# Kernel optimization log

Measured on AMD Instinct MI355X. Metric: run time of the kernel, lower is better.

## Reference

```python
import jax, jax.numpy as jnp
import numpy as np

B, D, N_CLASSES = 8192, 128, 50


def setup_inputs() -> dict:
    key = jax.random.key(0)
    k1, k2, k3 = jax.random.split(key, 3)
    anchor = jax.random.normal(k1, (B, D), dtype=jnp.float32)
    target = jax.random.normal(k2, (B, D), dtype=jnp.float32)
    labels = jax.random.randint(k3, (B,), 0, N_CLASSES)
    return {"anchor": anchor, "target": target, "labels": labels}


def reference(anchor, target, labels):
    # Faithful vectorization of QuadrupletLoss.nt_xent_loss.
    # Note: the original hardcodes temperature 0.05 (ignores self.temp).
    TEMP = 0.05
    n = labels.shape[0]
    diff = labels[:, None] != labels[None, :]                      # mask2: [B,B]
    same_off = (labels[:, None] == labels[None, :]) & ~jnp.eye(n, dtype=bool)  # mask

    # d[j, m] = <anchor[j], target[m]> / 0.05
    d = jnp.matmul(anchor, target.T) / TEMP                        # [B,B]
    neg = jnp.where(diff, d, -jnp.inf)
    mx = jax.lax.stop_gradient(jnp.max(neg, axis=1))               # maxdot.detach() per j
    mx = jnp.where(jnp.isfinite(mx), mx, 0.0)
    # s[j] = sum_{m: labels[m]!=labels[j]} exp(d[j,m] - mx[j])  (exp(-inf)=0 masks out)
    s = jnp.sum(jnp.exp(neg - mx[:, None]), axis=1)                # [B]

    # Inner double loop: nds[i] = sum over j with labels[j]!=labels[i] of s[j]
    difff = diff.astype(s.dtype)
    nds = difff @ s                                                # [B]
    negcount = jnp.sum(difff, axis=1)                              # negtivesum

    x = jnp.where(negcount > 0, nds / jnp.where(negcount > 0, negcount, 1.0), nds)
    log_prob = -jnp.log(x + 1e-12)                                 # constant across cols
    mask_sum = jnp.sum(same_off, axis=1)
    # (mask * log_prob).sum(1) / clamp(mask_sum,1) == log_prob where mask_sum>0 else 0
    pos_logits = jnp.where(mask_sum > 0, log_prob, 0.0)
    return -jnp.mean(pos_logits)
```

## Files before the change

### kernel.cpp

```cpp
#include <hip/hip_runtime.h>
#include <float.h>
#include <math.h>

typedef __attribute__((ext_vector_type(8))) short short8;
typedef __attribute__((ext_vector_type(8))) _Float16 half8;
typedef __attribute__((ext_vector_type(4))) float f32x4;

constexpr int B_N  = 8192;
constexpr int D_KK = 128;
constexpr int NCLS = 50;
constexpr int NCHUNK = 16;
constexpr int CCOLS = B_N / NCHUNK;
constexpr int NPBLK = 32;
constexpr float C_SCALE = 28.853900817779268f;
constexpr float THR = 40.0f;
constexpr float NEG_LOW  = -1.0e5f;
constexpr float NEG_MASK = -1.0e30f;

__device__ __forceinline__ float exp2fast(float x) { return __builtin_amdgcn_exp2f(x); }

__global__ void prep_kernel(const float* __restrict__ a, const float* __restrict__ b,
                            short* __restrict__ aH, short* __restrict__ bT)
{
    const int NPER = B_N * D_KK / 8;
    int i = blockIdx.x * blockDim.x + threadIdx.x;
    if (i < NPER) {
        const f32x4* sp = (const f32x4*)(a + (size_t)i * 8);
        f32x4 v0 = sp[0], v1 = sp[1];
        short8 h;
#pragma unroll
        for (int e = 0; e < 4; ++e) {
            h[e]     = __builtin_bit_cast(short, (_Float16)(C_SCALE * v0[e]));
            h[e + 4] = __builtin_bit_cast(short, (_Float16)(C_SCALE * v1[e]));
        }
        *(short8*)(aH + (size_t)i * 8) = h;
    } else {
        int j   = i - NPER;
        int kq  = j & 15;
        int col = j >> 4;
        const f32x4* sp = (const f32x4*)(b + (size_t)col * D_KK + kq * 8);
        f32x4 v0 = sp[0], v1 = sp[1];
        short8 h;
#pragma unroll
        for (int e = 0; e < 4; ++e) {
            h[e]     = __builtin_bit_cast(short, (_Float16)v0[e]);
            h[e + 4] = __builtin_bit_cast(short, (_Float16)v1[e]);
        }
        *(short8*)(bT + (size_t)kq * B_N * 8 + (size_t)col * 8) = h;
    }
}

__global__ __launch_bounds__(256)
void rowstats_kernel(const short* __restrict__ aH, const short* __restrict__ bT,
                     const int* __restrict__ labels,
                     float* __restrict__ pmx, float* __restrict__ ps)
{
    const int bid   = blockIdx.x;
    const int chunk = bid & (NCHUNK - 1);
    const int R0    = (bid >> 4) * 128;
    const int C0    = chunk * CCOLS;

    const int tid = threadIdx.x;
    const int wid = tid >> 6, l = tid & 63;
    const int l15 = l & 15, l16 = l >> 4;
    const int wrow = R0 + wid * 32;

    half8 aF[2][4];
#pragma unroll
    for (int mf = 0; mf < 2; ++mf) {
        const int arow = wrow + mf * 16 + l15;
#pragma unroll
        for (int ks = 0; ks < 4; ++ks)
            aF[mf][ks] = __builtin_bit_cast(half8,
                *(const short8*)(aH + (size_t)arow * D_KK + ks * 32 + l16 * 8));
    }

    int labA[8];
#pragma unroll
    for (int mf = 0; mf < 2; ++mf)
#pragma unroll
        for (int r = 0; r < 4; ++r)
            labA[mf * 4 + r] = labels[wrow + mf * 16 + l16 * 4 + r];

    float mxr[8], sm[8], ref[8];
#pragma unroll
    for (int i = 0; i < 8; ++i) { mxr[i] = NEG_LOW; sm[i] = 0.0f; ref[i] = 0.0f; }

    const char* cb = (const char*)(bT + (size_t)C0 * 8);
    int vo[2][4];
#pragma unroll
    for (int nf = 0; nf < 2; ++nf)
#pragma unroll
        for (int ks = 0; ks < 4; ++ks)
            vo[nf][ks] = ((ks * 4 + l16) * B_N + nf * 16 + l15) * 16;

    const int NT = CCOLS / 32;

    half8 bF[2][4];
#pragma unroll
    for (int nf = 0; nf < 2; ++nf)
#pragma unroll
        for (int ks = 0; ks < 4; ++ks)
            bF[nf][ks] = __builtin_bit_cast(half8, *(const short8*)(cb + vo[nf][ks]));

#pragma unroll 1
    for (int t = 0; t < NT; ++t) {
        f32x4 acc[2][2];
#pragma unroll
        for (int mf = 0; mf < 2; ++mf)
#pragma unroll
            for (int nf = 0; nf < 2; ++nf)
#pragma unroll
                for (int r = 0; r < 4; ++r) acc[mf][nf][r] = -ref[mf * 4 + r];

#pragma unroll
        for (int ks = 0; ks < 4; ++ks)
#pragma unroll
            for (int mf = 0; mf < 2; ++mf)
#pragma unroll
                for (int nf = 0; nf < 2; ++nf)
                    acc[mf][nf] = __builtin_amdgcn_mfma_f32_16x16x32_f16(
                        aF[mf][ks], bF[nf][ks], acc[mf][nf], 0, 0, 0);

        if (t + 1 < NT) {
            const int off = (t + 1) * 512;
#pragma unroll
            for (int nf = 0; nf < 2; ++nf)
#pragma unroll
                for (int ks = 0; ks < 4; ++ks)
                    bF[nf][ks] = __builtin_bit_cast(half8,
                        *(const short8*)(cb + vo[nf][ks] + off));
        }

        const int colB = C0 + t * 32;
        const int lB0 = labels[colB + l15];
        const int lB1 = labels[colB + 16 + l15];

        float vm0[8], vm1[8];
        int trig = 0;
#pragma unroll
        for (int mf = 0; mf < 2; ++mf)
#pragma unroll
            for (int r = 0; r < 4; ++r) {
                const int i = mf * 4 + r;
                float v0 = (lB0 != labA[i]) ? acc[mf][0][r] : NEG_MASK;
                float v1 = (lB1 != labA[i]) ? acc[mf][1][r] : NEG_MASK;
                mxr[i] = fmaxf(fmaxf(mxr[i], v0), v1);
                vm0[i] = v0; vm1[i] = v1;
                trig |= (mxr[i] > THR) ? 1 : 0;
            }
        if (__any(trig)) {
#pragma unroll
            for (int i = 0; i < 8; ++i) {
                float dlt = fmaxf(mxr[i], 0.0f);
                sm[i] *= exp2fast(-dlt);
                ref[i] += dlt; mxr[i] -= dlt;
                vm0[i] -= dlt; vm1[i] -= dlt;
            }
        }
#pragma unroll
        for (int i = 0; i < 8; ++i)
            sm[i] += exp2fast(vm0[i]) + exp2fast(vm1[i]);
    }

    float mxa[8], so[8];
#pragma unroll
    for (int i = 0; i < 8; ++i) {
        mxa[i] = ref[i] + mxr[i];
        so[i]  = sm[i] * exp2fast(fminf(-mxr[i], 126.0f));
    }
#pragma unroll
    for (int i = 0; i < 8; ++i) {
#pragma unroll
        for (int off = 1; off < 16; off <<= 1) {
            float m2 = __shfl_xor(mxa[i], off);
            float s2 = __shfl_xor(so[i], off);
            float nm = fmaxf(mxa[i], m2);
            so[i] = so[i] * exp2fast(mxa[i] - nm) + s2 * exp2fast(m2 - nm);
            mxa[i] = nm;
        }
    }
    if (l15 == 0) {
#pragma unroll
        for (int mf = 0; mf < 2; ++mf)
#pragma unroll
            for (int r = 0; r < 4; ++r) {
                int row = wrow + mf * 16 + l16 * 4 + r;
                pmx[chunk * B_N + row] = mxa[mf * 4 + r];
                ps [chunk * B_N + row] = so[mf * 4 + r];
            }
    }
}

__global__ void classsum_kernel(const float* __restrict__ pmx, const float* __restrict__ ps,
                                const int* __restrict__ labels,
                                float* __restrict__ partSum, unsigned int* __restrict__ partCnt)
{
    __shared__ float        csL[NCLS];
    __shared__ unsigned int ccL[NCLS];
    int t = threadIdx.x;
    if (t < NCLS) { csL[t] = 0.0f; ccL[t] = 0u; }
    __syncthreads();

    int j = blockIdx.x * blockDim.x + t;
    float m = -FLT_MAX, s = 0.0f;
#pragma unroll 4
    for (int c = 0; c < NCHUNK; ++c) {
        float m2 = pmx[(size_t)c * B_N + j];
        float s2 = ps [(size_t)c * B_N + j];
        float nm = fmaxf(m, m2);
        s = s * exp2fast(m - nm) + s2 * exp2fast(m2 - nm);
        m = nm;
    }
    int lab = labels[j];
    atomicAdd(&csL[lab], s);
    atomicAdd(&ccL[lab], 1u);
    __syncthreads();
    if (t < NCLS) {
        partSum[blockIdx.x * NCLS + t] = csL[t];
        partCnt[blockIdx.x * NCLS + t] = ccL[t];
    }
}

__global__ void loss_kernel(const float* __restrict__ partSum,
                            const unsigned int* __restrict__ partCnt,
                            float* __restrict__ out)
{
    int c = threadIdx.x;
    float cs = 0.0f;
    unsigned int cc = 0u;
    if (c < NCLS) {
#pragma unroll 4
        for (int b = 0; b < NPBLK; ++b) {
            cs += partSum[b * NCLS + c];
            cc += partCnt[b * NCLS + c];
        }
    }

    float tot = cs;
#pragma unroll
    for (int off = 1; off < 64; off <<= 1) tot += __shfl_xor(tot, off);

    float contrib = 0.0f;
    if (c < NCLS && cc > 0u) {
        float negc = (float)(B_N - (int)cc);
        float nds  = tot - cs;
        float x    = (negc > 0.0f) ? (nds / negc) : nds;
        float lp   = (cc >= 2u) ? (-logf(x + 1e-12f)) : 0.0f;
        contrib = (float)cc * lp;
    }
#pragma unroll
    for (int off = 1; off < 64; off <<= 1) contrib += __shfl_xor(contrib, off);
    if (c == 0) out[0] = -(contrib / (float)B_N);
}

extern "C" void kernel_launch(void* const* d_in, const int* in_sizes, int n_in,
                              void* d_out, int out_size, void* d_ws, size_t ws_size,
                              hipStream_t stream)
{
    const float* anchor = (const float*)d_in[0];
    const float* target = (const float*)d_in[1];
    const int*   labels = (const int*)d_in[2];
    float* out = (float*)d_out;

    const size_t PLANE = (size_t)B_N * D_KK * sizeof(short);
    char* ws = (char*)d_ws;
    short* aH = (short*)(ws + 0 * PLANE);
    short* bT = (short*)(ws + 1 * PLANE);
    float* ps  = (float*)(ws + 2 * PLANE);
    float* pmx = (float*)(ws + 2 * PLANE + sizeof(float) * NCHUNK * B_N);
    char*  cls = ws + 2 * PLANE + 2 * sizeof(float) * NCHUNK * B_N;
    float*        partSum = (float*)cls;
    unsigned int* partCnt = (unsigned int*)(cls + NPBLK * NCLS * sizeof(float));

    prep_kernel<<<2 * (B_N * D_KK / 8) / 256, 256, 0, stream>>>(anchor, target, aH, bT);
    rowstats_kernel<<<(B_N / 128) * NCHUNK, 256, 0, stream>>>(aH, bT, labels, pmx, ps);
    classsum_kernel<<<B_N / 256, 256, 0, stream>>>(pmx, ps, labels, partSum, partCnt);
    loss_kernel<<<1, 64, 0, stream>>>(partSum, partCnt, out);
}
```

Measured before the change: 54.60 us.

## Fold label mask into GEMM via one-hot augmented K dimension

The K dimension grows from 128 to 192 by appending a one-hot label block: anchor rows carry -4096 at their label's slot and target columns carry 1.0, so same-label dot products are pushed far negative by the MFMA itself. This removes the per-tile label loads and compare/select masking in the rowstats loop. The running rescale offset now seeds the MFMA accumulator as a bias, the column loop is partially unrolled, and the final merge becomes a max reduction followed by a sum reduction. The cost is 50% more MFMA work and B-tile loads per tile, plus more prep work and a larger workspace.

```diff
diff --git a/kernel.cpp b/kernel.cpp
--- a/kernel.cpp
+++ b/kernel.cpp
@@ -7,52 +7,76 @@
 typedef __attribute__((ext_vector_type(4))) float f32x4;
 
 constexpr int B_N  = 8192;
-constexpr int D_KK = 128;
+constexpr int D_K  = 128;
+constexpr int K_AUG = 192;
+constexpr int NKQ  = K_AUG / 8;
 constexpr int NCLS = 50;
 constexpr int NCHUNK = 16;
-constexpr int CCOLS = B_N / NCHUNK;
+constexpr int CCOLS = 512;
 constexpr int NPBLK = 32;
 constexpr float C_SCALE = 28.853900817779268f;
-constexpr float THR = 40.0f;
-constexpr float NEG_LOW  = -1.0e5f;
-constexpr float NEG_MASK = -1.0e30f;
+constexpr float PEN  = 4096.0f;
+constexpr float THR  = 40.0f;
+constexpr float NEG_LOW = -1.0e5f;
 
 __device__ __forceinline__ float exp2fast(float x) { return __builtin_amdgcn_exp2f(x); }
 
 __global__ void prep_kernel(const float* __restrict__ a, const float* __restrict__ b,
+                            const int* __restrict__ labels,
                             short* __restrict__ aH, short* __restrict__ bT)
 {
-    const int NPER = B_N * D_KK / 8;
+    const int NA = B_N * NKQ;
     int i = blockIdx.x * blockDim.x + threadIdx.x;
-    if (i < NPER) {
-        const f32x4* sp = (const f32x4*)(a + (size_t)i * 8);
-        f32x4 v0 = sp[0], v1 = sp[1];
+    if (i < NA) {
+        int row = i / NKQ, kq = i - row * NKQ;
         short8 h;
-#pragma unroll
-        for (int e = 0; e < 4; ++e) {
-            h[e]     = __builtin_bit_cast(short, (_Float16)(C_SCALE * v0[e]));
-            h[e + 4] = __builtin_bit_cast(short, (_Float16)(C_SCALE * v1[e]));
-        }
-        *(short8*)(aH + (size_t)i * 8) = h;
-    } else {
-        int j   = i - NPER;
-        int kq  = j & 15;
-        int col = j >> 4;
-        const f32x4* sp = (const f32x4*)(b + (size_t)col * D_KK + kq * 8);
-        f32x4 v0 = sp[0], v1 = sp[1];
-        short8 h;
-#pragma unroll
-        for (int e = 0; e < 4; ++e) {
-            h[e]     = __builtin_bit_cast(short, (_Float16)v0[e]);
-            h[e + 4] = __builtin_bit_cast(short, (_Float16)v1[e]);
-        }
-        *(short8*)(bT + (size_t)kq * B_N * 8 + (size_t)col * 8) = h;
+        if (kq < 16) {
+            const f32x4* sp = (const f32x4*)(a + (size_t)row * D_K + kq * 8);
+            f32x4 v0 = sp[0], v1 = sp[1];
+#pragma unroll
+            for (int e = 0; e < 4; ++e) {
+                h[e]     = __builtin_bit_cast(short, (_Float16)(C_SCALE * v0[e]));
+                h[e + 4] = __builtin_bit_cast(short, (_Float16)(C_SCALE * v1[e]));
+            }
+        } else {
+            int lab = labels[row];
+            int base = (kq - 16) * 8;
+#pragma unroll
+            for (int e = 0; e < 8; ++e)
+                h[e] = __builtin_bit_cast(short, (lab == base + e) ? (_Float16)(-PEN)
+                                                                   : (_Float16)0.0f);
+        }
+        *(short8*)(aH + (size_t)row * K_AUG + kq * 8) = h;
+    } else if (i < NA + B_N) {
+        int col = i - NA;
+        int lab = labels[col];
+#pragma unroll 4
+        for (int kq = 0; kq < 16; ++kq) {
+            const f32x4* sp = (const f32x4*)(b + (size_t)col * D_K + kq * 8);
+            f32x4 v0 = sp[0], v1 = sp[1];
+            short8 h;
+#pragma unroll
+            for (int e = 0; e < 4; ++e) {
+                h[e]     = __builtin_bit_cast(short, (_Float16)v0[e]);
+                h[e + 4] = __builtin_bit_cast(short, (_Float16)v1[e]);
+            }
+            *(short8*)(bT + ((size_t)kq * B_N + col) * 8) = h;
+        }
+#pragma unroll
+        for (int kq = 16; kq < 24; ++kq) {
+            int base = (kq - 16) * 8;
+            short8 h;
+#pragma unroll
+            for (int e = 0; e < 8; ++e)
+                h[e] = __builtin_bit_cast(short, (lab == base + e) ? (_Float16)1.0f
+                                                                   : (_Float16)0.0f);
+            *(short8*)(bT + ((size_t)kq * B_N + col) * 8) = h;
+        }
     }
 }
 
 __global__ __launch_bounds__(256)
 void rowstats_kernel(const short* __restrict__ aH, const short* __restrict__ bT,
-                     const int* __restrict__ labels,
                      float* __restrict__ pmx, float* __restrict__ ps)
 {
     const int bid   = blockIdx.x;
@@ -65,130 +89,114 @@
     const int l15 = l & 15, l16 = l >> 4;
     const int wrow = R0 + wid * 32;
 
-    half8 aF[2][4];
+    half8 aF[2][6];
 #pragma unroll
     for (int mf = 0; mf < 2; ++mf) {
         const int arow = wrow + mf * 16 + l15;
 #pragma unroll
-        for (int ks = 0; ks < 4; ++ks)
+        for (int ks = 0; ks < 6; ++ks)
             aF[mf][ks] = __builtin_bit_cast(half8,
-                *(const short8*)(aH + (size_t)arow * D_KK + ks * 32 + l16 * 8));
-    }
-
-    int labA[8];
-#pragma unroll
-    for (int mf = 0; mf < 2; ++mf)
-#pragma unroll
-        for (int r = 0; r < 4; ++r)
-            labA[mf * 4 + r] = labels[wrow + mf * 16 + l16 * 4 + r];
-
-    float mxr[8], sm[8], ref[8];
-#pragma unroll
-    for (int i = 0; i < 8; ++i) { mxr[i] = NEG_LOW; sm[i] = 0.0f; ref[i] = 0.0f; }
-
-    const char* cb = (const char*)(bT + (size_t)C0 * 8);
-    int vo[2][4];
+                *(const short8*)(aH + (size_t)arow * K_AUG + ks * 32 + l16 * 8));
+    }
+
+    float mxr[8], sm[8];
+    f32x4 bias[2];
+#pragma unroll
+    for (int i = 0; i < 8; ++i) { mxr[i] = NEG_LOW; sm[i] = 0.0f; }
+    bias[0] = f32x4{0.f, 0.f, 0.f, 0.f};
+    bias[1] = f32x4{0.f, 0.f, 0.f, 0.f};
+
+    const char* cb = (const char*)bT + (size_t)C0 * 16;
+    int vo[2][6];
 #pragma unroll
     for (int nf = 0; nf < 2; ++nf)
 #pragma unroll
-        for (int ks = 0; ks < 4; ++ks)
+        for (int ks = 0; ks < 6; ++ks)
             vo[nf][ks] = ((ks * 4 + l16) * B_N + nf * 16 + l15) * 16;
 
-    const int NT = CCOLS / 32;
-
-    half8 bF[2][4];
+    half8 bF[2][6];
 #pragma unroll
     for (int nf = 0; nf < 2; ++nf)
 #pragma unroll
-        for (int ks = 0; ks < 4; ++ks)
+        for (int ks = 0; ks < 6; ++ks)
             bF[nf][ks] = __builtin_bit_cast(half8, *(const short8*)(cb + vo[nf][ks]));
 
-#pragma unroll 1
-    for (int t = 0; t < NT; ++t) {
-        f32x4 acc[2][2];
-#pragma unroll
-        for (int mf = 0; mf < 2; ++mf)
-#pragma unroll
-            for (int nf = 0; nf < 2; ++nf)
-#pragma unroll
-                for (int r = 0; r < 4; ++r) acc[mf][nf][r] = -ref[mf * 4 + r];
-
-#pragma unroll
-        for (int ks = 0; ks < 4; ++ks)
+    for (int tt = 0; tt < 4; ++tt) {
+        const char* cbt = cb + tt * 2048;
+#pragma unroll
+        for (int ti = 0; ti < 4; ++ti) {
+            f32x4 acc[2][2];
 #pragma unroll
             for (int mf = 0; mf < 2; ++mf)
 #pragma unroll
                 for (int nf = 0; nf < 2; ++nf)
                     acc[mf][nf] = __builtin_amdgcn_mfma_f32_16x16x32_f16(
-                        aF[mf][ks], bF[nf][ks], acc[mf][nf], 0, 0, 0);
-
-        if (t + 1 < NT) {
-            const int off = (t + 1) * 512;
-#pragma unroll
-            for (int nf = 0; nf < 2; ++nf)
-#pragma unroll
-                for (int ks = 0; ks < 4; ++ks)
-                    bF[nf][ks] = __builtin_bit_cast(half8,
-                        *(const short8*)(cb + vo[nf][ks] + off));
-        }
-
-        const int colB = C0 + t * 32;
-        const int lB0 = labels[colB + l15];
-        const int lB1 = labels[colB + 16 + l15];
-
-        float vm0[8], vm1[8];
-        int trig = 0;
-#pragma unroll
-        for (int mf = 0; mf < 2; ++mf)
-#pragma unroll
-            for (int r = 0; r < 4; ++r) {
-                const int i = mf * 4 + r;
-                float v0 = (lB0 != labA[i]) ? acc[mf][0][r] : NEG_MASK;
-                float v1 = (lB1 != labA[i]) ? acc[mf][1][r] : NEG_MASK;
-                mxr[i] = fmaxf(fmaxf(mxr[i], v0), v1);
-                vm0[i] = v0; vm1[i] = v1;
-                trig |= (mxr[i] > THR) ? 1 : 0;
-            }
-        if (__any(trig)) {
+                        aF[mf][0], bF[nf][0], bias[mf], 0, 0, 0);
+#pragma unroll
+            for (int ks = 1; ks < 6; ++ks)
+#pragma unroll
+                for (int mf = 0; mf < 2; ++mf)
+#pragma unroll
+                    for (int nf = 0; nf < 2; ++nf)
+                        acc[mf][nf] = __builtin_amdgcn_mfma_f32_16x16x32_f16(
+                            aF[mf][ks], bF[nf][ks], acc[mf][nf], 0, 0, 0);
+
+            if (!(tt == 3 && ti == 3)) {
+#pragma unroll
+                for (int nf = 0; nf < 2; ++nf)
+#pragma unroll
+                    for (int ks = 0; ks < 6; ++ks)
+                        bF[nf][ks] = __builtin_bit_cast(half8,
+                            *(const short8*)(cbt + vo[nf][ks] + (ti + 1) * 512));
+            }
+
+            float v0[8], v1[8], nmx[8];
+#pragma unroll
+            for (int mf = 0; mf < 2; ++mf)
+#pragma unroll
+                for (int r = 0; r < 4; ++r) {
+                    const int i = mf * 4 + r;
+                    v0[i] = acc[mf][0][r];
+                    v1[i] = acc[mf][1][r];
+                    nmx[i] = fmaxf(fmaxf(mxr[i], v0[i]), v1[i]);
+                }
+            float tmax = fmaxf(fmaxf(fmaxf(nmx[0], nmx[1]), fmaxf(nmx[2], nmx[3])),
+                               fmaxf(fmaxf(nmx[4], nmx[5]), fmaxf(nmx[6], nmx[7])));
+            if (__any(tmax > THR)) {
+#pragma unroll
+                for (int mf = 0; mf < 2; ++mf)
+#pragma unroll
+                    for (int r = 0; r < 4; ++r) {
+                        const int i = mf * 4 + r;
+                        float dlt = fmaxf(nmx[i], 0.0f);
+                        sm[i] *= exp2fast(-dlt);
+                        bias[mf][r] -= dlt;
+                        nmx[i] -= dlt; v0[i] -= dlt; v1[i] -= dlt;
+                    }
+            }
 #pragma unroll
             for (int i = 0; i < 8; ++i) {
-                float dlt = fmaxf(mxr[i], 0.0f);
-                sm[i] *= exp2fast(-dlt);
-                ref[i] += dlt; mxr[i] -= dlt;
-                vm0[i] -= dlt; vm1[i] -= dlt;
-            }
-        }
-#pragma unroll
-        for (int i = 0; i < 8; ++i)
-            sm[i] += exp2fast(vm0[i]) + exp2fast(vm1[i]);
-    }
-
-    float mxa[8], so[8];
+                sm[i] += exp2fast(v0[i]) + exp2fast(v1[i]);
+                mxr[i] = nmx[i];
+            }
+        }
+    }
+
 #pragma unroll
     for (int i = 0; i < 8; ++i) {
-        mxa[i] = ref[i] + mxr[i];
-        so[i]  = sm[i] * exp2fast(fminf(-mxr[i], 126.0f));
-    }
-#pragma unroll
-    for (int i = 0; i < 8; ++i) {
-#pragma unroll
-        for (int off = 1; off < 16; off <<= 1) {
-            float m2 = __shfl_xor(mxa[i], off);
-            float s2 = __shfl_xor(so[i], off);
-            float nm = fmaxf(mxa[i], m2);
-            so[i] = so[i] * exp2fast(mxa[i] - nm) + s2 * exp2fast(m2 - nm);
-            mxa[i] = nm;
-        }
-    }
-    if (l15 == 0) {
-#pragma unroll
-        for (int mf = 0; mf < 2; ++mf)
-#pragma unroll
-            for (int r = 0; r < 4; ++r) {
-                int row = wrow + mf * 16 + l16 * 4 + r;
-                pmx[chunk * B_N + row] = mxa[mf * 4 + r];
-                ps [chunk * B_N + row] = so[mf * 4 + r];
-            }
+        float ref = -bias[i >> 2][i & 3];
+        float mxa = ref + mxr[i];
+        float m = mxa;
+#pragma unroll
+        for (int off = 1; off < 16; off <<= 1) m = fmaxf(m, __shfl_xor(m, off));
+        float so = sm[i] * exp2fast(fminf(ref - m, 100.0f));
+#pragma unroll
+        for (int off = 1; off < 16; off <<= 1) so += __shfl_xor(so, off);
+        if (l15 == 0) {
+            int row = wrow + (i >> 2) * 16 + l16 * 4 + (i & 3);
+            pmx[chunk * B_N + row] = m;
+            ps [chunk * B_N + row] = so;
+        }
     }
 }
 
@@ -263,7 +271,7 @@
     const int*   labels = (const int*)d_in[2];
     float* out = (float*)d_out;
 
-    const size_t PLANE = (size_t)B_N * D_KK * sizeof(short);
+    const size_t PLANE = (size_t)B_N * K_AUG * sizeof(short);
     char* ws = (char*)d_ws;
     short* aH = (short*)(ws + 0 * PLANE);
     short* bT = (short*)(ws + 1 * PLANE);
@@ -273,8 +281,9 @@
     float*        partSum = (float*)cls;
     unsigned int* partCnt = (unsigned int*)(cls + NPBLK * NCLS * sizeof(float));
 
-    prep_kernel<<<2 * (B_N * D_KK / 8) / 256, 256, 0, stream>>>(anchor, target, aH, bT);
-    rowstats_kernel<<<(B_N / 128) * NCHUNK, 256, 0, stream>>>(aH, bT, labels, pmx, ps);
+    const int nprep = B_N * NKQ + B_N;
+    prep_kernel<<<nprep / 256, 256, 0, stream>>>(anchor, target, labels, aH, bT);
+    rowstats_kernel<<<(B_N / 128) * NCHUNK, 256, 0, stream>>>(aH, bT, pmx, ps);
     classsum_kernel<<<B_N / 256, 256, 0, stream>>>(pmx, ps, labels, partSum, partCnt);
     loss_kernel<<<1, 64, 0, stream>>>(partSum, partCnt, out);
 }
```

Measured after the change: 73.79 us. +35.1%, slower.
